# Kernel tuning notes

Hardware: AMD Instinct MI355X
Metric: run time of the kernel (lower is better)

Reference implementation:

```python
import jax, jax.numpy as jnp
import numpy as np
from jax import lax

BASE_SIZE = 16.0
FEAT_STRIDE = 16
RATIOS = (0.5, 1.0, 2.0)
SCALES = (8.0, 16.0, 32.0)
N_PRE_NMS = 6000   # eval-mode ProposalCreator defaults
N_POST_NMS = 300
NMS_THRESH = 0.7
MIN_SIZE = 16.0
SCALE = 1.0


def anchor_base():
    # generate_anchor_base: loops ratio-major, scale-minor -> 9 anchors (y1,x1,y2,x2)
    r = jnp.asarray(RATIOS, jnp.float32)
    s = jnp.asarray(SCALES, jnp.float32)
    h = (BASE_SIZE * s[None, :] * jnp.sqrt(r)[:, None]).reshape(-1)
    w = (BASE_SIZE * s[None, :] * jnp.sqrt(1.0 / r)[:, None]).reshape(-1)
    c = BASE_SIZE / 2.0
    return jnp.stack([c - h / 2, c - w / 2, c + h / 2, c + w / 2], axis=1)  # [9,4]


def enumerate_anchors(hh, ww):
    # replicates _enumerate_shift_anchor incl. torch.meshgrid(shift_x, shift_y) 'ij' ordering
    sy = jnp.arange(hh, dtype=jnp.float32) * FEAT_STRIDE
    sx = jnp.arange(ww, dtype=jnp.float32) * FEAT_STRIDE
    gx, gy = jnp.meshgrid(sx, sy, indexing='ij')  # shapes [ww, hh]
    shift = jnp.stack([gy.ravel(), gx.ravel(), gy.ravel(), gx.ravel()], axis=1)  # [K,4]
    a = anchor_base()[None, :, :] + shift[:, None, :]  # [K,9,4]
    return a.reshape(-1, 4)


def conv2d(x, w, b, pad):
    y = lax.conv_general_dilated(x, w, (1, 1), [(pad, pad), (pad, pad)],
                                 dimension_numbers=('NCHW', 'OIHW', 'NCHW'))
    return y + b[None, :, None, None]


def loc2bbox(anchor, loc):
    h = anchor[:, 2] - anchor[:, 0]
    w = anchor[:, 3] - anchor[:, 1]
    cy = anchor[:, 0] + 0.5 * h
    cx = anchor[:, 1] + 0.5 * w
    dy, dx, dh, dw = loc[:, 0], loc[:, 1], loc[:, 2], loc[:, 3]
    cy = dy * h + cy
    cx = dx * w + cx
    h = jnp.exp(dh) * h
    w = jnp.exp(dw) * w
    return jnp.stack([cy - 0.5 * h, cx - 0.5 * w, cy + 0.5 * h, cx + 0.5 * w], axis=1)


def propose(loc, score, anchor, img_h, img_w):
    # ProposalCreator for a single image: decode, clip, min-size filter, top-k, NMS, pad to N_POST_NMS
    roi = loc2bbox(anchor, loc)
    roi = jnp.stack([jnp.clip(roi[:, 0], 0.0, img_h), jnp.clip(roi[:, 1], 0.0, img_w),
                     jnp.clip(roi[:, 2], 0.0, img_h), jnp.clip(roi[:, 3], 0.0, img_w)], axis=1)
    ms = MIN_SIZE * SCALE
    valid = ((roi[:, 2] - roi[:, 0]) >= ms) & ((roi[:, 3] - roi[:, 1]) >= ms)
    score = jnp.where(valid, score, -jnp.inf)
    top_s, order = lax.top_k(score, N_PRE_NMS)          # score-descending candidates
    boxes = roi[order]                                   # [N_PRE,4]
    valid_s = top_s > -jnp.inf
    # pairwise IoU [N_PRE,N_PRE]
    area = (boxes[:, 2] - boxes[:, 0]) * (boxes[:, 3] - boxes[:, 1])
    tl = jnp.maximum(boxes[:, None, :2], boxes[None, :, :2])
    br = jnp.minimum(boxes[:, None, 2:], boxes[None, :, 2:])
    inter = jnp.prod(jnp.clip(br - tl, 0.0, None), axis=-1)
    iou = lax.stop_gradient(inter / (area[:, None] + area[None, :] - inter))
    idxs = jnp.arange(N_PRE_NMS)
    def body(keep, i):
        sup = (iou[i] > NMS_THRESH) & (idxs > i) & keep[i]
        return keep & ~sup, None
    keep, _ = lax.scan(body, valid_s, idxs)              # greedy NMS over score-sorted boxes
    # kept indices in score order (stable argsort: True(kept) sorts first as 0)
    sel = jnp.argsort(jnp.logical_not(keep))[:N_POST_NMS]
    out_valid = jnp.arange(N_POST_NMS) < jnp.sum(keep)
    return jnp.where(out_valid[:, None], boxes[sel], 0.0)  # [N_POST,4], zero-padded


def rpn_forward(x, conv1_w, conv1_b, score_w, score_b, loc_w, loc_b, img_h, img_w):
    n, _, hh, ww = x.shape
    anchor = enumerate_anchors(hh, ww)                   # [hh*ww*9, 4]
    A = anchor.shape[0] // (hh * ww)
    feat = jax.nn.relu(conv2d(x, conv1_w, conv1_b, 1))   # [n,512,hh,ww]
    locs = conv2d(feat, loc_w, loc_b, 0).transpose(0, 2, 3, 1).reshape(n, -1, 4)
    raw_scores = conv2d(feat, score_w, score_b, 0).transpose(0, 2, 3, 1)  # [n,hh,ww,A*2]
    fg = jax.nn.softmax(raw_scores.reshape(n, hh, ww, A, 2), axis=4)[..., 1].reshape(n, -1)
    scores = raw_scores.reshape(n, -1, 2)
    rois = jax.vmap(lambda l, s: propose(l, s, anchor, float(img_h), float(img_w)))(locs, fg)
    roi_indices = jnp.broadcast_to(jnp.arange(n, dtype=jnp.int32)[:, None], (n, N_POST_NMS))
    return locs, scores, rois, roi_indices, anchor


def setup_inputs() -> dict:
    key = jax.random.key(0)
    ks = jax.random.split(key, 4)
    x = jax.random.normal(ks[0], (4, 512, 50, 50), jnp.float32)
    conv1_w = jax.random.normal(ks[1], (512, 512, 3, 3), jnp.float32) * 0.01
    conv1_b = jnp.zeros((512,), jnp.float32)
    score_w = jax.random.normal(ks[2], (18, 512, 1, 1), jnp.float32) * 0.01
    score_b = jnp.zeros((18,), jnp.float32)
    loc_w = jax.random.normal(ks[3], (36, 512, 1, 1), jnp.float32) * 0.01
    loc_b = jnp.zeros((36,), jnp.float32)
    return {'x': x, 'conv1_w': conv1_w, 'conv1_b': conv1_b, 'score_w': score_w,
            'score_b': score_b, 'loc_w': loc_w, 'loc_b': loc_b, 'img_h': 800, 'img_w': 800}


def reference(x, conv1_w, conv1_b, score_w, score_b, loc_w, loc_b, img_h, img_w):
    return rpn_forward(x, conv1_w, conv1_b, score_w, score_b, loc_w, loc_b, img_h, img_w)
```

## Files before the change

### kernel.cpp

```cpp
#include <hip/hip_runtime.h>
#include <stdint.h>

#define NB 4
#define CIN 512
#define PIX 2500
#define KTOT 4608
#define NBOX 22500
#define NPRE 6000
#define NPOST 300
#define NWORD 94
#define SCAP 8192

#define O_LOCS   0
#define O_SCORES 360000
#define O_ROIS   540000
#define O_RIDX   544800
#define O_ANCH   546000

#define XT_ROWS 2960
#define XT_FRONT 64
#define XT_IMG (XT_ROWS * 512)
#define XT_SPLIT_BYTES ((size_t)NB * XT_IMG * 2)

#define WO_XT1   0ull
#define WO_XT2   12124160ull
#define WO_WSBLK 24248320ull
#define WO_FEATP 33685504ull
#define WO_WT    74645504ull
#define WO_BOXES 74760192ull
#define WO_DKEY  76200192ull
#define WO_BOX6K 76560192ull
#define WO_VALID 76944192ull
#define WO_MASK  0ull

#define FEATP_HALF 5120000

typedef _Float16 h8 __attribute__((ext_vector_type(8)));
typedef float f32x4 __attribute__((ext_vector_type(4)));
typedef unsigned int u32;
typedef unsigned long long u64;

__device__ __forceinline__ void gll16(const void* g, void* l) {
  __builtin_amdgcn_global_load_lds((const __attribute__((address_space(1))) u32*)g,
                                   (__attribute__((address_space(3))) u32*)l, 16, 0, 0);
}

__device__ __forceinline__ float rd_dim(const int* p) {
  int v = *p;
  if (v > 0 && v < 1000000) return (float)v;
  return __int_as_float(v);
}

__global__ void k_zero(u32* __restrict__ xt) {
  size_t n = (2 * XT_SPLIT_BYTES) / 4;
  for (size_t i = blockIdx.x * 256ull + threadIdx.x; i < n; i += (size_t)gridDim.x * 256)
    xt[i] = 0u;
}

__global__ void k_xT(const float* __restrict__ x, _Float16* __restrict__ x1,
                     _Float16* __restrict__ x2) {
  __shared__ float sx[3200];
  int chunk = blockIdx.x, r0 = blockIdx.y, b = blockIdx.z;
  int t = threadIdx.x;
  int ic0 = chunk * 64;
  for (int i = t; i < 3200; i += 256) {
    int icl = i / 50, c = i - icl * 50;
    sx[i] = x[(((size_t)b * 512 + ic0 + icl) * 50 + r0) * 50 + c];
  }
  __syncthreads();
  for (int j = t; j < 3200; j += 256) {
    int c = j >> 6, icl = j & 63;
    float v = sx[icl * 50 + c];
    _Float16 h1 = (_Float16)v;
    _Float16 h2 = (_Float16)(v - (float)h1);
    size_t dst = (size_t)b * XT_IMG + (size_t)(XT_FRONT + (r0 + 1) * 52 + (c + 1)) * 512 + ic0 + icl;
    x1[dst] = h1;
    x2[dst] = h2;
  }
}

__global__ void k_splitw(const float* __restrict__ w, _Float16* __restrict__ wblk) {
  int n = 4 * 144 * 16 * 512;
  for (int idx = blockIdx.x * 256 + threadIdx.x; idx < n; idx += gridDim.x * 256) {
    int lane8 = idx & 511;
    int l = lane8 >> 3, j = lane8 & 7;
    int reg = (idx >> 9) & 15;
    int t = idx >> 13;
    int ksI = t % 144, mt = t / 144;
    int ocs = reg >> 1, s = reg & 1;
    int oc = mt * 128 + ocs * 16 + (l & 15);
    int k = ksI * 32 + (l >> 4) * 8 + j;
    int tap = k >> 9, ic = k & 511;
    float v = w[((size_t)oc * 512 + ic) * 9 + tap];
    _Float16 h1 = (_Float16)v;
    wblk[idx] = s ? (_Float16)(v - (float)h1) : h1;
  }
}

__global__ void k_wt(const float* __restrict__ loc_w, const float* __restrict__ score_w,
                     float* __restrict__ wt) {
  int idx = blockIdx.x * 256 + threadIdx.x;
  if (idx >= 128 * 56 * 4) return;
  int i = idx & 3, j = (idx >> 2) % 56, c4 = idx / 224;
  int c = c4 * 4 + i;
  float v = 0.f;
  if (j < 36) v = loc_w[(size_t)j * 512 + c];
  else if (j < 54) v = score_w[(size_t)(j - 36) * 512 + c];
  wt[idx] = v;
}

__global__ __launch_bounds__(128, 2) void k_conv(
    const _Float16* __restrict__ xs1, const _Float16* __restrict__ xs2,
    const _Float16* __restrict__ wsBlk,
    float* __restrict__ featP) {
  __shared__ _Float16 lds[16384];
  int id = blockIdx.x;
  int bz = id & 7;
  int inner = id >> 3;
  int st = inner / 44;
  int idx2 = inner - st * 44;
  int nt = idx2 >> 1;
  int mt = st * 2 + (idx2 & 1);
  int b = bz >> 1, ks = bz & 1;
  int t = threadIdx.x, lane = t & 63, w = t >> 6;
  int mb = mt * 128, nb = nt * 128;
  int l15 = lane & 15, l4 = lane >> 4;
  const _Float16* xi1 = xs1 + (size_t)b * XT_IMG + (size_t)XT_FRONT * 512;
  const _Float16* xi2 = xs2 + (size_t)b * XT_IMG + (size_t)XT_FRONT * 512;
  const _Float16* wbase = wsBlk + ((size_t)(mt * 144 + ks * 72) * 16 + w * 8) * 512 + lane * 8;

  f32x4 acc[4][8];
#pragma unroll
  for (int i = 0; i < 4; i++)
#pragma unroll
    for (int j = 0; j < 8; j++)
      acc[i][j] = (f32x4){0.f, 0.f, 0.f, 0.f};

  auto stageB = [&](int kk, int off) {
    int kg = ks * 2304 + kk * 32;
    int tap = kg >> 9, ic0 = kg & 511;
    int sh = (tap / 3 - 1) * 52 + (tap % 3) - 1;
#pragma unroll
    for (int u = 0; u < 8; u++) {
      int r = w * 8 + u;
      int pxs = r >> 1, s = r & 1;
      const _Float16* xp = s ? xi2 : xi1;
      int qp = nb + pxs * 16 + l15 + sh;
      gll16(xp + (ptrdiff_t)qp * 512 + ic0 + l4 * 8, &lds[off + r * 512]);
    }
  };
  auto loadA = [&](int kk, h8* a) {
    const _Float16* p = wbase + (size_t)kk * 16 * 512;
#pragma unroll
    for (int u = 0; u < 8; u++) a[u] = *(const h8*)(p + u * 512);
  };
  auto compute = [&](int off, const h8* a) {
#pragma unroll
    for (int nf = 0; nf < 8; nf++) {
      h8 b0 = *(const h8*)&lds[off + (nf * 2 + 0) * 512 + lane * 8];
      h8 b1 = *(const h8*)&lds[off + (nf * 2 + 1) * 512 + lane * 8];
      __builtin_amdgcn_s_setprio(1);
#pragma unroll
      for (int mf = 0; mf < 4; mf++) {
        acc[mf][nf] = __builtin_amdgcn_mfma_f32_16x16x32_f16(a[mf * 2 + 0], b0, acc[mf][nf], 0, 0, 0);
        acc[mf][nf] = __builtin_amdgcn_mfma_f32_16x16x32_f16(a[mf * 2 + 0], b1, acc[mf][nf], 0, 0, 0);
        acc[mf][nf] = __builtin_amdgcn_mfma_f32_16x16x32_f16(a[mf * 2 + 1], b0, acc[mf][nf], 0, 0, 0);
      }
      __builtin_amdgcn_s_setprio(0);
    }
  };

  h8 aA[8], aB[8];
  loadA(0, aA);
  stageB(0, 0);
  __syncthreads();
#pragma unroll 1
  for (int kp = 0; kp < 36; kp++) {
    int kk = 2 * kp;
    stageB(kk + 1, 8192);
    loadA(kk + 1, aB);
    compute(0, aA);
    __syncthreads();
    if (kp < 35) {
      stageB(kk + 2, 0);
      loadA(kk + 2, aA);
    }
    compute(8192, aB);
    __syncthreads();
  }

  float* fp = featP + (size_t)ks * FEATP_HALF;
#pragma unroll
  for (int nf = 0; nf < 8; nf++) {
    int q = nb + nf * 16 + l15;
    int r = q / 52, c = q - r * 52;
    if (r >= 1 && r <= 50 && c >= 1 && c <= 50) {
      int p = (r - 1) * 50 + (c - 1);
      size_t base = ((size_t)b * PIX + p) * 512;
#pragma unroll
      for (int mf = 0; mf < 4; mf++) {
        int oc0 = mb + w * 64 + mf * 16 + l4 * 4;
        *(float4*)&fp[base + oc0] = make_float4(acc[mf][nf][0], acc[mf][nf][1],
                                                acc[mf][nf][2], acc[mf][nf][3]);
      }
    }
  }
}

__global__ __launch_bounds__(256) void k_heads(const float* __restrict__ featP,
                                               const float* __restrict__ wt4,
                                               const float* __restrict__ conv_b,
                                               const float* __restrict__ loc_b,
                                               const float* __restrict__ score_b,
                                               const int* __restrict__ ihp,
                                               const int* __restrict__ iwp,
                                               float* __restrict__ out,
                                               float* __restrict__ boxes,
                                               uint32_t* __restrict__ dkey) {
  __shared__ float swt[16 * 56 * 4];
  int wv = threadIdx.x >> 6;
  int wid = blockIdx.x * 4 + wv;
  int lane = threadIdx.x & 63;
  int b = wid / PIX, p = wid % PIX;
  int row = lane < 54 ? lane : 54;
  const float* f0 = featP + ((size_t)b * PIX + p) * 512;
  const float* f1 = f0 + FEATP_HALF;
  float acc = 0.f;
  for (int cc = 0; cc < 8; cc++) {
    __syncthreads();
    for (int j = threadIdx.x; j < 16 * 224; j += 256)
      swt[j] = wt4[(size_t)cc * 16 * 224 + j];
    __syncthreads();
#pragma unroll 4
    for (int cl = 0; cl < 16; cl++) {
      int c4 = cc * 16 + cl;
      float4 u = *(const float4*)(f0 + c4 * 4);
      float4 v = *(const float4*)(f1 + c4 * 4);
      float4 bb = *(const float4*)(conv_b + c4 * 4);
      float4 wvv = *(const float4*)(&swt[(cl * 56 + row) * 4]);
      acc += fmaxf(u.x + v.x + bb.x, 0.f) * wvv.x;
      acc += fmaxf(u.y + v.y + bb.y, 0.f) * wvv.y;
      acc += fmaxf(u.z + v.z + bb.z, 0.f) * wvv.z;
      acc += fmaxf(u.w + v.w + bb.w, 0.f) * wvv.w;
    }
  }
  float bi = 0.f;
  if (lane < 36) bi = loc_b[lane];
  else if (lane < 54) bi = score_b[lane - 36];
  acc += bi;
  if (lane < 36) out[O_LOCS + (size_t)b * 90000 + (size_t)p * 36 + lane] = acc;
  else if (lane < 54) out[O_SCORES + (size_t)b * 45000 + (size_t)p * 18 + (lane - 36)] = acc;

  float imgH = rd_dim(ihp), imgW = rd_dim(iwp);
  int gy = p % 50, gx = p / 50;
  float sy = 16.f * gy, sx = 16.f * gx;

  int a9 = (lane < 9) ? lane : 0;
  float dy  = __shfl(acc, a9 * 4 + 0);
  float dxv = __shfl(acc, a9 * 4 + 1);
  float dh  = __shfl(acc, a9 * 4 + 2);
  float dw  = __shfl(acc, a9 * 4 + 3);
  float l0  = __shfl(acc, 36 + a9 * 2);
  float l1  = __shfl(acc, 36 + a9 * 2 + 1);

  {
    float rr = (a9 < 3) ? 0.5f : (a9 < 6 ? 1.f : 2.f);
    int si = a9 % 3;
    float ssc = (si == 0) ? 8.f : (si == 1 ? 16.f : 32.f);
    float hb = 16.f * ssc * sqrtf(rr);
    float wb = 16.f * ssc * sqrtf(1.f / rr);
    float ay1 = (8.f - hb * 0.5f) + sy;
    float ax1 = (8.f - wb * 0.5f) + sx;
    float ay2 = (8.f + hb * 0.5f) + sy;
    float ax2 = (8.f + wb * 0.5f) + sx;
    float h = ay2 - ay1, w2d = ax2 - ax1;
    float cy = ay1 + 0.5f * h, cx = ax1 + 0.5f * w2d;
    float cy2 = dy * h + cy, cx2 = dxv * w2d + cx;
    float h2 = expf(dh) * h, ww2 = expf(dw) * w2d;
    float y1 = cy2 - 0.5f * h2, x1 = cx2 - 0.5f * ww2;
    float y2 = cy2 + 0.5f * h2, x2 = cx2 + 0.5f * ww2;
    y1 = fminf(fmaxf(y1, 0.f), imgH);
    x1 = fminf(fmaxf(x1, 0.f), imgW);
    y2 = fminf(fmaxf(y2, 0.f), imgH);
    x2 = fminf(fmaxf(x2, 0.f), imgW);
    bool valid = (y2 - y1 >= 16.f) && (x2 - x1 >= 16.f);
    float m = fmaxf(l0, l1);
    float e0 = expf(l0 - m), e1 = expf(l1 - m);
    float fg = e1 / (e0 + e1);
    float scv = valid ? fg : -INFINITY;
    if (lane < 9) {
      size_t k = (size_t)b * NBOX + (size_t)p * 9 + a9;
      *(float4*)(boxes + k * 4) = make_float4(y1, x1, y2, x2);
      uint32_t u = __float_as_uint(scv);
      uint32_t f2 = (u >> 31) ? ~u : (u | 0x80000000u);
      dkey[k] = ~f2;
    }
  }
  if (b == 0 && lane < 36) {
    int aa = lane >> 2, dd = lane & 3;
    float rr2 = (aa < 3) ? 0.5f : (aa < 6 ? 1.f : 2.f);
    int si2 = aa % 3;
    float ss2 = (si2 == 0) ? 8.f : (si2 == 1 ? 16.f : 32.f);
    float hb2 = 16.f * ss2 * sqrtf(rr2);
    float wb2 = 16.f * ss2 * sqrtf(1.f / rr2);
    float v;
    if (dd == 0) v = (8.f - hb2 * 0.5f) + sy;
    else if (dd == 1) v = (8.f - wb2 * 0.5f) + sx;
    else if (dd == 2) v = (8.f + hb2 * 0.5f) + sy;
    else v = (8.f + wb2 * 0.5f) + sx;
    out[O_ANCH + (size_t)p * 36 + lane] = v;
  }
}

__global__ void k_topk(const uint32_t* __restrict__ dkey, const float* __restrict__ boxes,
                       float* __restrict__ box6k,
                       unsigned long long* __restrict__ validm) {
  extern __shared__ char smem[];
  u64* cand = (u64*)smem;
  u64* alt  = (u64*)(smem + 65536);
  u32* hcnt = (u32*)(smem + 131072);
  u32* wc     = (u32*)(smem + 139264);
  u32* digTot = wc + 16;
  u32* digBase = digTot + 16;
  u32* msc = digBase + 16;
  u32* histw = (u32*)(smem + 65536);
  u32* hist = histw + 4096;
  int b = blockIdx.x, tid = threadIdx.x;
  int wq = tid >> 6, l = tid & 63;
  const uint32_t* dk = dkey + (size_t)b * NBOX;

  uint32_t P = 0, need = NPRE;
  for (int pass = 0; pass < 4; pass++) {
    int sh = 24 - 8 * pass;
    for (int i = tid; i < 16 * 256; i += 1024) histw[i] = 0;
    __syncthreads();
    for (int i = tid; i < NBOX; i += 1024) {
      uint32_t d = dk[i];
      bool match = (((uint64_t)d >> (sh + 8)) == ((uint64_t)P >> (sh + 8)));
      if (match) atomicAdd(&histw[wq * 256 + ((d >> sh) & 255u)], 1u);
    }
    __syncthreads();
    for (int bin = tid; bin < 256; bin += 1024) {
      uint32_t s = 0;
#pragma unroll
      for (int q = 0; q < 16; q++) s += histw[q * 256 + bin];
      hist[bin] = s;
    }
    __syncthreads();
    if (tid < 64) {
      uint32_t h0 = hist[l * 4 + 0], h1 = hist[l * 4 + 1];
      uint32_t h2 = hist[l * 4 + 2], h3 = hist[l * 4 + 3];
      uint32_t p1 = h0, p2 = h0 + h1, p3 = p2 + h2, p4 = p3 + h3;
      uint32_t s = p4;
#pragma unroll
      for (int dd = 1; dd < 64; dd <<= 1) { uint32_t v = __shfl_up(s, dd); if (l >= dd) s += v; }
      uint32_t excl = s - p4;
      uint32_t i0 = excl + p1, i1 = excl + p2, i2 = excl + p3, i3 = excl + p4;
      int local = 4;
      if (i0 >= need) local = 0;
      else if (i1 >= need) local = 1;
      else if (i2 >= need) local = 2;
      else if (i3 >= need) local = 3;
      u64 bal = __ballot(local < 4);
      int lw = bal ? __builtin_ctzll(bal) : 63;
      if (l == lw) {
        if (local < 4) {
          msc[0] = (uint32_t)(l * 4 + local);
          msc[1] = (local == 0) ? excl : (local == 1) ? i0 : (local == 2) ? i1 : i2;
        } else {
          msc[0] = 255u;
          msc[1] = i2;
        }
      }
    }
    __syncthreads();
    need -= msc[1];
    P |= msc[0] << sh;
    __syncthreads();
  }
  uint32_t Dstar = P;

  if (tid == 0) msc[2] = 0;
  __syncthreads();
  for (int c = 0; c < 22; c++) {
    int i = c * 1024 + tid;
    uint32_t d = (i < NBOX) ? dk[i] : 0xFFFFFFFFu;
    bool pred = (i < NBOX) && (d <= Dstar);
    u64 bal = __ballot(pred);
    uint32_t rank = (uint32_t)__popcll(bal & ((1ull << l) - 1ull));
    __syncthreads();
    if (l == 0) wc[wq] = (uint32_t)__popcll(bal);
    __syncthreads();
    if (tid < 64) {
      uint32_t v = (l < 16) ? wc[l] : 0u;
      uint32_t s = v;
#pragma unroll
      for (int dd = 1; dd < 16; dd <<= 1) { uint32_t t2 = __shfl_up(s, dd); if (l >= dd) s += t2; }
      uint32_t base0 = msc[2];
      if (l < 16) wc[l] = base0 + s - v;
      if (l == 15) msc[2] = base0 + s;
    }
    __syncthreads();
    if (pred) {
      uint32_t pos = wc[wq] + rank;
      if (pos < SCAP) cand[pos] = ((u64)d << 32) | (uint32_t)i;
    }
  }
  __syncthreads();
  uint32_t cnt = msc[2] < SCAP ? msc[2] : SCAP;
  for (int i = (int)cnt + tid; i < SCAP; i += 1024) cand[i] = ~0ull;
  __syncthreads();

  u64* src = cand;
  u64* dst = alt;
  for (int pass = 0; pass < 8; pass++) {
    int sh = 32 + pass * 4;
    for (int i = tid; i < 2048; i += 1024) hcnt[i] = 0;
    __syncthreads();
    for (int c = 0; c < 8; c++) {
      int i = c * 1024 + tid;
      uint32_t dig = (uint32_t)(src[i] >> sh) & 15u;
      u64 m = ~0ull;
#pragma unroll
      for (int bit = 0; bit < 4; bit++) {
        u64 bb = __ballot((dig >> bit) & 1u);
        m &= ((dig >> bit) & 1u) ? bb : ~bb;
      }
      if (l == __builtin_ctzll(m)) hcnt[(i >> 6) * 16 + dig] = (uint32_t)__popcll(m);
    }
    __syncthreads();
    {
      int d = wq;
      uint32_t cl = hcnt[l * 16 + d];
      uint32_t ch = hcnt[(l + 64) * 16 + d];
      uint32_t s = cl;
#pragma unroll
      for (int dd = 1; dd < 64; dd <<= 1) { uint32_t v = __shfl_up(s, dd); if (l >= dd) s += v; }
      uint32_t tl = __shfl(s, 63);
      uint32_t el = s - cl;
      uint32_t s2 = ch;
#pragma unroll
      for (int dd = 1; dd < 64; dd <<= 1) { uint32_t v = __shfl_up(s2, dd); if (l >= dd) s2 += v; }
      uint32_t th = __shfl(s2, 63);
      uint32_t eh = tl + (s2 - ch);
      hcnt[l * 16 + d] = el;
      hcnt[(l + 64) * 16 + d] = eh;
      if (l == 0) digTot[d] = tl + th;
    }
    __syncthreads();
    if (tid == 0) {
      uint32_t basev = 0;
      for (int d2 = 0; d2 < 16; d2++) { digBase[d2] = basev; basev += digTot[d2]; }
    }
    __syncthreads();
    for (int c = 0; c < 8; c++) {
      int i = c * 1024 + tid;
      u64 key = src[i];
      uint32_t dig = (uint32_t)(key >> sh) & 15u;
      u64 m = ~0ull;
#pragma unroll
      for (int bit = 0; bit < 4; bit++) {
        u64 bb = __ballot((dig >> bit) & 1u);
        m &= ((dig >> bit) & 1u) ? bb : ~bb;
      }
      uint32_t rank = (uint32_t)__popcll(m & ((1ull << l) - 1ull));
      uint32_t dpos = digBase[dig] + hcnt[(i >> 6) * 16 + dig] + rank;
      dst[dpos] = key;
    }
    __syncthreads();
    u64* tmp = src; src = dst; dst = tmp;
  }

  for (int r = tid; r < NPRE; r += 1024) {
    u64 kk = cand[r];
    uint32_t idx = (uint32_t)kk;
    float4 bx = *(const float4*)(boxes + ((size_t)b * NBOX + idx) * 4);
    *(float4*)(box6k + ((size_t)b * NPRE + r) * 4) = bx;
  }
  for (int wi = tid; wi < NWORD; wi += 1024) {
    unsigned long long m = 0ull;
    for (int bb = 0; bb < 64; bb++) {
      int r = wi * 64 + bb;
      if (r < NPRE) {
        uint32_t d = (uint32_t)(cand[r] >> 32);
        if (d < 0xFF800000u) m |= (1ull << bb);
      }
    }
    validm[b * NWORD + wi] = m;
  }
}

__global__ __launch_bounds__(256) void k_mask(const float* __restrict__ box6k,
                                              unsigned long long* __restrict__ mask) {
  int b = blockIdx.z, it = blockIdx.x, wt = blockIdx.y;
  int t = threadIdx.x;
  int il = t & 31, wl = t >> 5;
  if (wt * 512 + 511 <= it * 32) return;
  __shared__ float bi[32][4];
  __shared__ float bj[512][4];
  if (t < 128) {
    int ii = it * 32 + (t >> 2);
    if (ii > NPRE - 1) ii = NPRE - 1;
    bi[t >> 2][t & 3] = box6k[((size_t)b * NPRE + ii) * 4 + (t & 3)];
  }
#pragma unroll
  for (int q = 0; q < 2; q++) {
    int v = t + 256 * q;
    int jg = wt * 512 + v;
    float4 f = make_float4(0.f, 0.f, 0.f, 0.f);
    if (jg < NPRE) f = *(const float4*)(box6k + ((size_t)b * NPRE + jg) * 4);
    *(float4*)&bj[v][0] = f;
  }
  __syncthreads();
  int i = it * 32 + il;
  int w = wt * 8 + wl;
  if (i >= NPRE || w >= NWORD) return;
  float y1 = bi[il][0], x1 = bi[il][1], y2 = bi[il][2], x2 = bi[il][3];
  float ar = (y2 - y1) * (x2 - x1);
  unsigned long long m = 0ull;
  int jbase = w * 64;
  for (int jj = 0; jj < 64; jj++) {
    int j = jbase + jj;
    int js = wl * 64 + jj;
    float jy1 = bj[js][0], jx1 = bj[js][1], jy2 = bj[js][2], jx2 = bj[js][3];
    float tlY = fmaxf(y1, jy1), tlX = fmaxf(x1, jx1);
    float brY = fminf(y2, jy2), brX = fminf(x2, jx2);
    float ih = fmaxf(brY - tlY, 0.f), iw2 = fmaxf(brX - tlX, 0.f);
    float inter = ih * iw2;
    float arj = (jy2 - jy1) * (jx2 - jx1);
    float iou = inter / (ar + arj - inter);
    if (iou > 0.7f && j > i && j < NPRE) m |= (1ull << jj);
  }
  mask[((size_t)b * NPRE + i) * NWORD + w] = m;
}

__global__ void k_scan(const unsigned long long* __restrict__ mask,
                       const unsigned long long* __restrict__ validm,
                       const float* __restrict__ box6k, float* __restrict__ out) {
  int b = blockIdx.x;
  int lane = threadIdx.x;
  const unsigned long long* mb = mask + (size_t)b * NPRE * NWORD;
  u64 a0 = (lane < NWORD) ? validm[b * NWORD + lane] : 0ull;
  u64 a1 = (lane + 64 < NWORD) ? validm[b * NWORD + lane + 64] : 0ull;
  __shared__ int keptIdx[NPOST];
  int cnt = 0;
  bool done = false;
  u64 rowCur = mb[(size_t)lane * NWORD + 0];
  u64 rowN1 = mb[(size_t)(64 + lane) * NWORD + 1];
  for (int w = 0; w < NWORD && !done; w++) {
    u64 rowN2 = 0ull;
    if (w + 2 < NWORD) {
      int i2 = (w + 2) * 64 + lane;
      if (i2 < NPRE) rowN2 = mb[(size_t)i2 * NWORD + (w + 2)];
    }
    u64 alive = (w < 64) ? __shfl(a0, w) : __shfl(a1, w - 64);
    if (alive) {
      u64 keep = 0ull;
      while (alive) {
        int q = __builtin_ctzll(alive);
        alive &= alive - 1;
        keep |= (1ull << q);
        if (lane == 0) keptIdx[cnt] = w * 64 + q;
        cnt++;
        if (cnt >= NPOST) { done = true; break; }
        alive &= ~__shfl(rowCur, q);
      }
      if (w < 64) { if (lane == w) a0 = 0ull; }
      else        { if (lane == w - 64) a1 = 0ull; }
      if (!done) {
        while (keep) {
          u64 or0 = 0ull, or1 = 0ull;
#pragma unroll
          for (int z = 0; z < 8; z++) {
            if (keep) {
              int q = __builtin_ctzll(keep);
              keep &= keep - 1;
              int ki = w * 64 + q;
              u64 m0 = (lane < NWORD && lane > w) ? mb[(size_t)ki * NWORD + lane] : 0ull;
              u64 m1 = (lane + 64 < NWORD && lane + 64 > w) ? mb[(size_t)ki * NWORD + 64 + lane] : 0ull;
              or0 |= m0;
              or1 |= m1;
            }
          }
          a0 &= ~or0;
          a1 &= ~or1;
        }
      }
    }
    rowCur = rowN1;
    rowN1 = rowN2;
  }
  __syncthreads();
  for (int r = lane; r < NPOST; r += 64) {
    float4 bx = make_float4(0.f, 0.f, 0.f, 0.f);
    if (r < cnt) bx = *(const float4*)(box6k + ((size_t)b * NPRE + keptIdx[r]) * 4);
    *(float4*)(out + O_ROIS + ((size_t)b * NPOST + r) * 4) = bx;
    out[O_RIDX + b * NPOST + r] = (float)b;
  }
}

extern "C" void kernel_launch(void* const* d_in, const int* in_sizes, int n_in,
                              void* d_out, int out_size, void* d_ws, size_t ws_size,
                              hipStream_t stream) {
  const float* x       = (const float*)d_in[0];
  const float* conv1_w = (const float*)d_in[1];
  const float* conv1_b = (const float*)d_in[2];
  const float* score_w = (const float*)d_in[3];
  const float* score_b = (const float*)d_in[4];
  const float* loc_w   = (const float*)d_in[5];
  const float* loc_b   = (const float*)d_in[6];
  const int* ihp = (const int*)d_in[7];
  const int* iwp = (const int*)d_in[8];
  float* out = (float*)d_out;
  char* ws = (char*)d_ws;
  _Float16* xt1 = (_Float16*)(ws + WO_XT1);
  _Float16* xt2 = (_Float16*)(ws + WO_XT2);
  _Float16* wsBlk = (_Float16*)(ws + WO_WSBLK);
  float* featP = (float*)(ws + WO_FEATP);
  float* wt    = (float*)(ws + WO_WT);
  float* boxes = (float*)(ws + WO_BOXES);
  uint32_t* dkey  = (uint32_t*)(ws + WO_DKEY);
  float* box6k = (float*)(ws + WO_BOX6K);
  unsigned long long* validm = (unsigned long long*)(ws + WO_VALID);
  unsigned long long* mask   = (unsigned long long*)(ws + WO_MASK);

  k_zero<<<2048, 256, 0, stream>>>((u32*)xt1);
  k_xT<<<dim3(8, 50, NB), 256, 0, stream>>>(x, xt1, xt2);
  k_splitw<<<2048, 256, 0, stream>>>(conv1_w, wsBlk);
  k_wt<<<(128 * 56 * 4 + 255) / 256, 256, 0, stream>>>(loc_w, score_w, wt);
  k_conv<<<704, 128, 0, stream>>>(xt1, xt2, wsBlk, featP);
  k_heads<<<2500, 256, 0, stream>>>(featP, wt, conv1_b, loc_b, score_b,
                                    ihp, iwp, out, boxes, dkey);
  int topk_lds = 65536 * 2 + 8192 + 512;
  hipFuncSetAttribute((const void*)k_topk, hipFuncAttributeMaxDynamicSharedMemorySize,
                      topk_lds);
  k_topk<<<NB, 1024, topk_lds, stream>>>(dkey, boxes, box6k, validm);
  dim3 gm(188, 12, NB);
  k_mask<<<gm, 256, 0, stream>>>(box6k, mask);
  k_scan<<<NB, 64, 0, stream>>>(mask, validm, box6k, out);
}
```

Baseline: 580.8 us.

## Stage conv weights via LDS with triple-buffered async loads and smaller N tile

The conv GEMM kernel now loads the weight (A) fragments into LDS with global-to-LDS loads instead of per-wave register loads. It uses a three-stage ring buffer with vmcnt-based waits and raw barriers in place of double-buffered __syncthreads. The N tile is halved from 128 to 64 pixels, which doubles the grid to 1408 blocks and cuts accumulator registers. LDS use rises to 72KB per block with launch bounds of 1 block per CU, so occupancy may drop while latency hiding and load balance should improve.

```diff
diff --git a/kernel.cpp b/kernel.cpp
--- a/kernel.cpp
+++ b/kernel.cpp
@@ -109,89 +109,100 @@
   wt[idx] = v;
 }
 
-__global__ __launch_bounds__(128, 2) void k_conv(
+#define CVMW12 asm volatile("s_waitcnt vmcnt(12)" ::: "memory")
+#define CVMW0  asm volatile("s_waitcnt vmcnt(0)" ::: "memory")
+#define CBAR   __builtin_amdgcn_s_barrier()
+__global__ __launch_bounds__(128, 1) void k_conv(
     const _Float16* __restrict__ xs1, const _Float16* __restrict__ xs2,
     const _Float16* __restrict__ wsBlk,
     float* __restrict__ featP) {
-  __shared__ _Float16 lds[16384];
+  extern __shared__ _Float16 lds[];
   int id = blockIdx.x;
   int bz = id & 7;
   int inner = id >> 3;
-  int st = inner / 44;
-  int idx2 = inner - st * 44;
+  int st = inner / 88;
+  int idx2 = inner - st * 88;
   int nt = idx2 >> 1;
   int mt = st * 2 + (idx2 & 1);
   int b = bz >> 1, ks = bz & 1;
   int t = threadIdx.x, lane = t & 63, w = t >> 6;
-  int mb = mt * 128, nb = nt * 128;
+  int nb = nt * 64;
   int l15 = lane & 15, l4 = lane >> 4;
   const _Float16* xi1 = xs1 + (size_t)b * XT_IMG + (size_t)XT_FRONT * 512;
   const _Float16* xi2 = xs2 + (size_t)b * XT_IMG + (size_t)XT_FRONT * 512;
-  const _Float16* wbase = wsBlk + ((size_t)(mt * 144 + ks * 72) * 16 + w * 8) * 512 + lane * 8;
-
-  f32x4 acc[4][8];
+  const _Float16* wkb = wsBlk + (size_t)(mt * 144 + ks * 72) * 16 * 512;
+
+  f32x4 acc[4][4];
 #pragma unroll
   for (int i = 0; i < 4; i++)
 #pragma unroll
-    for (int j = 0; j < 8; j++)
+    for (int j = 0; j < 4; j++)
       acc[i][j] = (f32x4){0.f, 0.f, 0.f, 0.f};
 
-  auto stageB = [&](int kk, int off) {
+  auto stage = [&](int kk, int bufE) {
     int kg = ks * 2304 + kk * 32;
     int tap = kg >> 9, ic0 = kg & 511;
     int sh = (tap / 3 - 1) * 52 + (tap % 3) - 1;
 #pragma unroll
-    for (int u = 0; u < 8; u++) {
-      int r = w * 8 + u;
-      int pxs = r >> 1, s = r & 1;
-      const _Float16* xp = s ? xi2 : xi1;
-      int qp = nb + pxs * 16 + l15 + sh;
-      gll16(xp + (ptrdiff_t)qp * 512 + ic0 + l4 * 8, &lds[off + r * 512]);
+    for (int u = 0; u < 12; u++) {
+      int r = w * 12 + u;
+      if (r < 16) {
+        gll16(wkb + ((size_t)kk * 16 + r) * 512 + lane * 8, &lds[bufE + r * 512]);
+      } else {
+        int j = r - 16;
+        int pxs = j >> 1, s = j & 1;
+        const _Float16* xp = s ? xi2 : xi1;
+        gll16(xp + (ptrdiff_t)(nb + pxs * 16 + l15 + sh) * 512 + ic0 + l4 * 8,
+              &lds[bufE + r * 512]);
+      }
     }
   };
-  auto loadA = [&](int kk, h8* a) {
-    const _Float16* p = wbase + (size_t)kk * 16 * 512;
-#pragma unroll
-    for (int u = 0; u < 8; u++) a[u] = *(const h8*)(p + u * 512);
+  auto compute = [&](int bufE) {
+    h8 af[8];
+#pragma unroll
+    for (int u = 0; u < 8; u++)
+      af[u] = *(const h8*)&lds[bufE + (w * 8 + u) * 512 + lane * 8];
+#pragma unroll
+    for (int nf = 0; nf < 4; nf++) {
+      h8 b0 = *(const h8*)&lds[bufE + (16 + nf * 2 + 0) * 512 + lane * 8];
+      h8 b1 = *(const h8*)&lds[bufE + (16 + nf * 2 + 1) * 512 + lane * 8];
+      __builtin_amdgcn_s_setprio(1);
+#pragma unroll
+      for (int mf = 0; mf < 4; mf++) {
+        acc[mf][nf] = __builtin_amdgcn_mfma_f32_16x16x32_f16(af[mf * 2 + 0], b0, acc[mf][nf], 0, 0, 0);
+        acc[mf][nf] = __builtin_amdgcn_mfma_f32_16x16x32_f16(af[mf * 2 + 0], b1, acc[mf][nf], 0, 0, 0);
+        acc[mf][nf] = __builtin_amdgcn_mfma_f32_16x16x32_f16(af[mf * 2 + 1], b0, acc[mf][nf], 0, 0, 0);
+      }
+      __builtin_amdgcn_s_setprio(0);
+    }
   };
-  auto compute = [&](int off, const h8* a) {
-#pragma unroll
-    for (int nf = 0; nf < 8; nf++) {
-      h8 b0 = *(const h8*)&lds[off + (nf * 2 + 0) * 512 + lane * 8];
-      h8 b1 = *(const h8*)&lds[off + (nf * 2 + 1) * 512 + lane * 8];
-      __builtin_amdgcn_s_setprio(1);
-#pragma unroll
-      for (int mf = 0; mf < 4; mf++) {
-        acc[mf][nf] = __builtin_amdgcn_mfma_f32_16x16x32_f16(a[mf * 2 + 0], b0, acc[mf][nf], 0, 0, 0);
-        acc[mf][nf] = __builtin_amdgcn_mfma_f32_16x16x32_f16(a[mf * 2 + 0], b1, acc[mf][nf], 0, 0, 0);
-        acc[mf][nf] = __builtin_amdgcn_mfma_f32_16x16x32_f16(a[mf * 2 + 1], b0, acc[mf][nf], 0, 0, 0);
-      }
-      __builtin_amdgcn_s_setprio(0);
-    }
-  };
-
-  h8 aA[8], aB[8];
-  loadA(0, aA);
-  stageB(0, 0);
-  __syncthreads();
+
+  stage(0, 0);
+  stage(1, 12288);
 #pragma unroll 1
-  for (int kp = 0; kp < 36; kp++) {
-    int kk = 2 * kp;
-    stageB(kk + 1, 8192);
-    loadA(kk + 1, aB);
-    compute(0, aA);
-    __syncthreads();
-    if (kp < 35) {
-      stageB(kk + 2, 0);
-      loadA(kk + 2, aA);
-    }
-    compute(8192, aB);
-    __syncthreads();
-  }
+  for (int kp = 0; kp < 23; kp++) {
+    int kk = 3 * kp;
+    CVMW12; CBAR;
+    stage(kk + 2, 24576);
+    compute(0);
+    CVMW12; CBAR;
+    stage(kk + 3, 0);
+    compute(12288);
+    CVMW12; CBAR;
+    stage(kk + 4, 12288);
+    compute(24576);
+  }
+  CVMW12; CBAR;
+  stage(71, 24576);
+  compute(0);
+  CVMW12; CBAR;
+  compute(12288);
+  CVMW0; CBAR;
+  compute(24576);
 
   float* fp = featP + (size_t)ks * FEATP_HALF;
 #pragma unroll
-  for (int nf = 0; nf < 8; nf++) {
+  for (int nf = 0; nf < 4; nf++) {
     int q = nb + nf * 16 + l15;
     int r = q / 52, c = q - r * 52;
     if (r >= 1 && r <= 50 && c >= 1 && c <= 50) {
@@ -199,7 +210,7 @@
       size_t base = ((size_t)b * PIX + p) * 512;
 #pragma unroll
       for (int mf = 0; mf < 4; mf++) {
-        int oc0 = mb + w * 64 + mf * 16 + l4 * 4;
+        int oc0 = mt * 128 + w * 64 + mf * 16 + l4 * 4;
         *(float4*)&fp[base + oc0] = make_float4(acc[mf][nf][0], acc[mf][nf][1],
                                                 acc[mf][nf][2], acc[mf][nf][3]);
       }
@@ -628,7 +639,9 @@
   k_xT<<<dim3(8, 50, NB), 256, 0, stream>>>(x, xt1, xt2);
   k_splitw<<<2048, 256, 0, stream>>>(conv1_w, wsBlk);
   k_wt<<<(128 * 56 * 4 + 255) / 256, 256, 0, stream>>>(loc_w, score_w, wt);
-  k_conv<<<704, 128, 0, stream>>>(xt1, xt2, wsBlk, featP);
+  hipFuncSetAttribute((const void*)k_conv, hipFuncAttributeMaxDynamicSharedMemorySize,
+                      73728);
+  k_conv<<<1408, 128, 73728, stream>>>(xt1, xt2, wsBlk, featP);
   k_heads<<<2500, 256, 0, stream>>>(featP, wt, conv1_b, loc_b, score_b,
                                     ihp, iwp, out, boxes, dkey);
   int topk_lds = 65536 * 2 + 8192 + 512;
```

New measurement: 720.5 us. +24.1%, slower.
